# Kernel optimization log

Measured on AMD Instinct MI355X. Metric: run time of the kernel, lower is better.

## Reference

```python
import jax, jax.numpy as jnp
import numpy as np
from jax import lax

IMAGE_SIZE = 512
MIN_LEVEL, MAX_LEVEL = 3, 7
NUM_SCALES = 3
RATIOS = (1.0, 0.5, 2.0)
BASE_SCALE = 4
PRE_NMS = 5000
POST_NMS = 100
IOU_THR = 0.5
SCORE_THR = 0.2
NUM_CLASSES = 90
BATCH = 8


def _anchors():
    """Multiscale anchors [N,4] in (y1,x1,y2,x2) pixel coords, N=49104 for 512."""
    all_boxes = []
    for level in range(MIN_LEVEL, MAX_LEVEL + 1):
        stride = 2 ** level
        feat = IMAGE_SIZE // stride
        cy = (np.arange(feat, dtype=np.float32) + 0.5) * stride
        cx = (np.arange(feat, dtype=np.float32) + 0.5) * stride
        yv, xv = np.meshgrid(cy, cx, indexing='ij')
        yv = yv.reshape(-1)
        xv = xv.reshape(-1)
        half = []  # (half_h, half_w) per anchor config, 9 per cell
        for i in range(NUM_SCALES):
            base = (2.0 ** (i / 3.0)) * stride * BASE_SCALE
            for r in RATIOS:
                half.append((base / np.sqrt(r) / 2.0, base * np.sqrt(r) / 2.0))
        half = np.asarray(half, dtype=np.float32)  # [9,2]
        boxes = np.stack([
            yv[:, None] - half[None, :, 0],
            xv[:, None] - half[None, :, 1],
            yv[:, None] + half[None, :, 0],
            xv[:, None] + half[None, :, 1],
        ], axis=-1)  # [feat*feat, 9, 4]
        all_boxes.append(boxes.reshape(-1, 4))
    return np.concatenate(all_boxes, axis=0).astype(np.float32)


def setup_inputs() -> dict:
    key = jax.random.key(0)
    k1, k2 = jax.random.split(key)
    n = 49104
    box_deltas = jax.random.normal(k1, (BATCH, n, 4), jnp.float32) * 0.1
    cls_logits = jax.random.normal(k2, (BATCH, n, NUM_CLASSES), jnp.float32)
    return {"box_deltas": box_deltas, "cls_logits": cls_logits}


def _decode(anchors, deltas):
    # Delta2Box with mean=None/std=None: standard (dy,dx,dh,dw) decode.
    ah = anchors[:, 2] - anchors[:, 0]
    aw = anchors[:, 3] - anchors[:, 1]
    acy = (anchors[:, 0] + anchors[:, 2]) * 0.5
    acx = (anchors[:, 1] + anchors[:, 3]) * 0.5
    dy, dx, dh, dw = deltas[..., 0], deltas[..., 1], deltas[..., 2], deltas[..., 3]
    cy = dy * ah + acy
    cx = dx * aw + acx
    h = jnp.exp(dh) * ah
    w = jnp.exp(dw) * aw
    return jnp.stack([cy - h * 0.5, cx - w * 0.5, cy + h * 0.5, cx + w * 0.5], axis=-1)


def _iou_one_many(box, boxes):
    yy1 = jnp.maximum(box[0], boxes[:, 0])
    xx1 = jnp.maximum(box[1], boxes[:, 1])
    yy2 = jnp.minimum(box[2], boxes[:, 2])
    xx2 = jnp.minimum(box[3], boxes[:, 3])
    inter = jnp.maximum(yy2 - yy1, 0.0) * jnp.maximum(xx2 - xx1, 0.0)
    a1 = (box[2] - box[0]) * (box[3] - box[1])
    a2 = (boxes[:, 2] - boxes[:, 0]) * (boxes[:, 3] - boxes[:, 1])
    return inter / (a1 + a2 - inter + 1e-8)


def _nms_single(boxes, scores):
    # Greedy NMS over K boxes, at most POST_NMS selections. boxes [K,4], scores [K].
    @jax.checkpoint
    def step(s, _):
        i = jnp.argmax(s)
        sc = s[i]
        b = boxes[i]
        valid = sc > SCORE_THR
        suppress = _iou_one_many(b, boxes) > IOU_THR  # includes self
        s = jnp.where(suppress, jnp.float32(-1.0), s)
        out_b = jnp.where(valid, b, jnp.zeros_like(b))
        out_s = jnp.where(valid, sc, jnp.float32(0.0))
        return s, (out_b, out_s)
    _, (sel_b, sel_s) = lax.scan(step, scores, None, length=POST_NMS)
    return sel_b, sel_s  # [POST,4], [POST]


def reference(box_deltas, cls_logits):
    anchors = jnp.asarray(_anchors())
    boxes = _decode(anchors, box_deltas)                      # [B,N,4]
    boxes = jnp.clip(boxes / jnp.float32(IMAGE_SIZE), 0.0, 1.0)
    scores = jax.nn.sigmoid(cls_logits)                       # [B,N,C]
    scores_t = jnp.swapaxes(scores, 1, 2)                     # [B,C,N]
    top_s, top_i = lax.top_k(scores_t, PRE_NMS)               # [B,C,K]
    B = boxes.shape[0]
    bidx = jnp.arange(B)[:, None, None]
    top_b = boxes[bidx, top_i]                                # [B,C,K,4]
    sel_b, sel_s = jax.vmap(jax.vmap(_nms_single))(top_b, top_s)  # [B,C,P,4],[B,C,P]
    cls_ids = jnp.broadcast_to(
        jnp.arange(NUM_CLASSES, dtype=jnp.float32)[None, :, None], sel_s.shape)
    flat_s = sel_s.reshape(B, -1)
    flat_b = sel_b.reshape(B, -1, 4)
    flat_c = cls_ids.reshape(B, -1)
    out_s, idx = lax.top_k(flat_s, POST_NMS)                  # combine over classes
    bi = jnp.arange(B)[:, None]
    out_b = flat_b[bi, idx]
    out_c = flat_c[bi, idx]
    valid = jnp.sum((out_s > 0).astype(jnp.int32), axis=1)
    return out_b, out_s, out_c, valid
```

## Files before the change

kernel.cpp:

```cpp
#include <hip/hip_runtime.h>
#include <math.h>


#define NANCH 49104
#define NB 8
#define NC 90
#define NBC 720
#define POSTN 100
#define T1CAP 512
#define WMAX 8
#define CHUNK 512
#define NCH 96
#define LCAP 32
#define EDGE 0.93f
#define PRECHK 2.0f


__device__ __forceinline__ float sigmoid_ref(float x) {
  if (x >= 0.0f) return __fdiv_rn(1.0f, __fadd_rn(1.0f, expf(-x)));
  float e = expf(x);
  return __fdiv_rn(e, __fadd_rn(1.0f, e));
}

__device__ __forceinline__ float iou_ref(float4 a, float4 b) {
  float yy1 = fmaxf(a.x, b.x);
  float xx1 = fmaxf(a.y, b.y);
  float yy2 = fminf(a.z, b.z);
  float xx2 = fminf(a.w, b.w);
  float ih = fmaxf(__fsub_rn(yy2, yy1), 0.0f);
  float iw = fmaxf(__fsub_rn(xx2, xx1), 0.0f);
  float inter = __fmul_rn(ih, iw);
  float a1 = __fmul_rn(__fsub_rn(a.z, a.x), __fsub_rn(a.w, a.y));
  float a2 = __fmul_rn(__fsub_rn(b.z, b.x), __fsub_rn(b.w, b.y));
  float den = __fadd_rn(__fsub_rn(__fadd_rn(a1, a2), inter), 1e-8f);
  return __fdiv_rn(inter, den);
}


__global__ __launch_bounds__(256) void k_anchors(float4* __restrict__ anchors,
                                                 unsigned int* __restrict__ gcnt,
                                                 unsigned int* __restrict__ oflow) {
  int n = blockIdx.x * 256 + threadIdx.x;
  if (n < NBC) { gcnt[n] = 0u; oflow[n] = 0u; }
  if (n >= NANCH) return;
  int l, off;
  if (n < 36864)      { l = 0; off = 0; }
  else if (n < 46080) { l = 1; off = 36864; }
  else if (n < 48384) { l = 2; off = 46080; }
  else if (n < 48960) { l = 3; off = 48384; }
  else                { l = 4; off = 48960; }
  int stride = 8 << l;
  int feat = 64 >> l;
  int r = n - off;
  int cell = r / 9, a = r - cell * 9;
  int iy = cell / feat, ix = cell - iy * feat;
  int isc = a / 3, ir = a - isc * 3;
  double base = exp2((double)isc / 3.0) * (double)stride * 4.0;
  double rt = (ir == 0) ? 1.0 : (ir == 1 ? 0.5 : 2.0);
  double sq = sqrt(rt);
  float hh = (float)(base / sq / 2.0);
  float hw = (float)(base * sq / 2.0);
  float cy = __fmul_rn(__fadd_rn((float)iy, 0.5f), (float)stride);
  float cx = __fmul_rn(__fadd_rn((float)ix, 0.5f), (float)stride);
  anchors[n] = make_float4(__fsub_rn(cy, hh), __fsub_rn(cx, hw),
                           __fadd_rn(cy, hh), __fadd_rn(cx, hw));
}


__global__ __launch_bounds__(256) void k_decode(const float4* __restrict__ deltas,
                                                const float4* __restrict__ anchors,
                                                float4* __restrict__ boxes) {
  int i = blockIdx.x * 256 + threadIdx.x;
  if (i >= NB * NANCH) return;
  int n = i % NANCH;
  float4 a = anchors[n];
  float4 d = deltas[i];
  float ah = __fsub_rn(a.z, a.x);
  float aw = __fsub_rn(a.w, a.y);
  float acy = __fmul_rn(__fadd_rn(a.x, a.z), 0.5f);
  float acx = __fmul_rn(__fadd_rn(a.y, a.w), 0.5f);
  float cy = __fadd_rn(__fmul_rn(d.x, ah), acy);
  float cx = __fadd_rn(__fmul_rn(d.y, aw), acx);
  float h = __fmul_rn(expf(d.z), ah);
  float w = __fmul_rn(expf(d.w), aw);
  float y1 = __fsub_rn(cy, __fmul_rn(h, 0.5f));
  float x1 = __fsub_rn(cx, __fmul_rn(w, 0.5f));
  float y2 = __fadd_rn(cy, __fmul_rn(h, 0.5f));
  float x2 = __fadd_rn(cx, __fmul_rn(w, 0.5f));
  const float inv = 0.001953125f;
  y1 = fminf(fmaxf(__fmul_rn(y1, inv), 0.0f), 1.0f);
  x1 = fminf(fmaxf(__fmul_rn(x1, inv), 0.0f), 1.0f);
  y2 = fminf(fmaxf(__fmul_rn(y2, inv), 0.0f), 1.0f);
  x2 = fminf(fmaxf(__fmul_rn(x2, inv), 0.0f), 1.0f);
  boxes[i] = make_float4(y1, x1, y2, x2);
}


__global__ __launch_bounds__(256) void k_scan(const float4* __restrict__ logits4,
                                              unsigned long long* __restrict__ gcand,
                                              unsigned int* __restrict__ gcnt,
                                              unsigned int* __restrict__ oflow) {
  int b = blockIdx.y;
  int ch = blockIdx.x;
  int n0 = ch * CHUNK;
  int rows = min(CHUNK, NANCH - n0);
  const float4* base = logits4 + ((size_t)b * NANCH + n0) * 90 / 4;
  int tot4 = rows * 90 / 4;
  int tid = threadIdx.x;

  __shared__ unsigned long long lc[NC * LCAP];
  __shared__ unsigned int lcnt[NC];
  for (int c = tid; c < NC; c += 256) lcnt[c] = 0u;
  __syncthreads();

  for (int e4 = tid; e4 < tot4; e4 += 1024) {
    float4 v[4];
#pragma unroll
    for (int k = 0; k < 4; k++) {
      int idx = e4 + k * 256;
      if (idx < tot4) v[k] = base[idx];
    }
#pragma unroll
    for (int k = 0; k < 4; k++) {
      int idx = e4 + k * 256;
      if (idx >= tot4) break;
      float xs[4] = {v[k].x, v[k].y, v[k].z, v[k].w};
#pragma unroll
      for (int j = 0; j < 4; j++) {
        float x = xs[j];
        if (x >= PRECHK) {
          float s = sigmoid_ref(x);
          if (s >= EDGE) {
            int e = idx * 4 + j;
            int r = e / 90, c = e - r * 90;
            unsigned int pos = atomicAdd(&lcnt[c], 1u);
            if (pos < LCAP) {
              int n = n0 + r;
              lc[c * LCAP + pos] =
                  ((unsigned long long)__float_as_uint(s) << 32) |
                  (unsigned int)(65535 - n);
            }
          }
        }
      }
    }
  }
  __syncthreads();

  if (tid < NC) {
    unsigned int cnt = lcnt[tid];
    int bc = b * NC + tid;
    if (cnt > LCAP) {
      atomicOr(&oflow[bc], 1u);
      cnt = LCAP;
    }
    if (cnt > 0) {
      unsigned int pos0 = atomicAdd(&gcnt[bc], cnt);
      for (unsigned int k = 0; k < cnt; k++) {
        unsigned int p = pos0 + k;
        if (p < T1CAP) gcand[(size_t)bc * T1CAP + p] = lc[tid * LCAP + k];
      }
    }
  }
}


__global__ __launch_bounds__(256) void k_nms_t1(
    const unsigned long long* __restrict__ gcand,
    const unsigned int* __restrict__ gcnt, const unsigned int* __restrict__ oflow,
    const float4* __restrict__ boxes, float* __restrict__ sel_s,
    float4* __restrict__ sel_b, int* __restrict__ flags) {
  int bc = blockIdx.x;
  int b = bc / NC;
  int tid = threadIdx.x;
  int lane = tid & 63;
  int wv = tid >> 6;

  __shared__ unsigned long long cand[T1CAP];
  __shared__ float4 cbox[T1CAP];
  __shared__ __align__(16) unsigned long long rowm[T1CAP][WMAX];
  __shared__ int s_seli[POSTN];
  __shared__ int s_nsel;

  unsigned int cnt = gcnt[bc];
  bool overflow = (cnt > (unsigned)T1CAP) || (oflow[bc] != 0u);
  int M = (int)min(cnt, (unsigned)T1CAP);
  for (int e = tid; e < T1CAP; e += 256)
    cand[e] = (e < M) ? gcand[(size_t)bc * T1CAP + e] : 0ull;
  if (tid == 0) s_nsel = 0;
  __syncthreads();

  int SN = (M <= 128) ? 128 : (M <= 256) ? 256 : 512;
  int np = SN >> 1;
  for (int k = 2; k <= SN; k <<= 1) {
    for (int j = k >> 1; j > 0; j >>= 1) {
      int t = tid;
      if (t < np) {
        int i = ((t & ~(j - 1)) << 1) | (t & (j - 1));
        int p = i | j;
        unsigned long long a = cand[i], bb = cand[p];
        bool up = ((i & k) == 0);
        if (up ? (a < bb) : (a > bb)) { cand[i] = bb; cand[p] = a; }
      }
      __syncthreads();
    }
  }

  for (int e = tid; e < T1CAP; e += 256) {
    if (e < M) {
      int n = 65535 - (int)(cand[e] & 0xFFFFull);
      cbox[e] = boxes[(size_t)b * NANCH + n];
    } else {
      cbox[e] = make_float4(0.0f, 0.0f, 0.0f, 0.0f);
    }
  }
  __syncthreads();

  int W = (M + 63) >> 6;

  for (int i = tid; i < M; i += 256) {
    float4 bi = cbox[i];
    int wi = i >> 6;
    unsigned int bl = (unsigned int)(i & 63);
#pragma unroll
    for (int w = 0; w < WMAX; w++) {
      unsigned long long acc = 0ull;
      if (w >= wi && w < W) {
        int jmax = min(64, M - (w << 6));
#pragma unroll 4
        for (int jj = 0; jj < jmax; jj++) {
          float4 bj = cbox[(w << 6) + jj];
          if (iou_ref(bj, bi) > 0.5f) acc |= (1ull << jj);
        }
        if (w == wi) acc &= (~0ull) << bl;
      }
      rowm[i][w] = acc;
    }
  }
  __syncthreads();

  if (wv == 0) {
    unsigned long long av[WMAX];
#pragma unroll
    for (int w = 0; w < WMAX; w++) {
      int lo = w << 6;
      av[w] = (M >= lo + 64) ? ~0ull
            : (M > lo ? ((1ull << (M - lo)) - 1ull) : 0ull);
    }
    int nsel = 0;
    int pidx = -1;
    unsigned long long pr[WMAX];
#pragma unroll
    for (int w = 0; w < WMAX; w++) pr[w] = 0ull;
    for (int p = 0; p < POSTN; p++) {
      int idx = -1;
#pragma unroll
      for (int w = 0; w < WMAX; w++) {
        if (idx < 0 && av[w] != 0ull)
          idx = (w << 6) + (__ffsll((unsigned long long)av[w]) - 1);
      }
      if (idx < 0) break;
      if (lane == 0) s_seli[p] = idx;
      nsel++;
      if (idx == pidx) {
#pragma unroll
        for (int w = 0; w < WMAX; w++) av[w] &= ~pr[w];
      } else {
        const ulonglong2* rp = (const ulonglong2*)(&rowm[idx][0]);
#pragma unroll
        for (int w = 0; w < 4; w++) {
          ulonglong2 rr = rp[w];
          av[2 * w] &= ~rr.x;
          av[2 * w + 1] &= ~rr.y;
        }
      }
      int nx = idx + 1;
      if (nx < M) {
        const ulonglong2* rp2 = (const ulonglong2*)(&rowm[nx][0]);
#pragma unroll
        for (int w = 0; w < 4; w++) {
          ulonglong2 rr = rp2[w];
          pr[2 * w] = rr.x;
          pr[2 * w + 1] = rr.y;
        }
        pidx = nx;
      } else {
        pidx = -1;
      }
    }
    if (lane == 0) s_nsel = nsel;
  }
  __syncthreads();

  int ns = s_nsel;
  bool bad = overflow || (ns < POSTN);
  if (tid == 0) flags[bc] = bad ? 1 : 0;
  if (bad) return;
  for (int p = tid; p < POSTN; p += 256) {
    int i = s_seli[p];
    float s0 = __uint_as_float((unsigned int)(cand[i] >> 32));
    float4 bx = cbox[i];
    bool valid = (s0 > 0.2f);
    sel_s[bc * POSTN + p] = valid ? s0 : 0.0f;
    sel_b[bc * POSTN + p] = valid ? bx : make_float4(0, 0, 0, 0);
  }
}


__global__ __launch_bounds__(256) void k_flagall(int* __restrict__ flags) {
  int i = blockIdx.x * 256 + threadIdx.x;
  if (i < NBC) flags[i] = 1;
}


template <int CAP, int RANK>
__global__ __launch_bounds__(256) void k_nms_fb(const float* __restrict__ logits,
                                                const float4* __restrict__ boxes,
                                                float* __restrict__ sel_s,
                                                float4* __restrict__ sel_b,
                                                const int* __restrict__ flags) {
  int bc = blockIdx.x;
  if (flags[bc] == 0) return;
  int b = bc / NC;
  int c = bc - b * NC;
  int tid = threadIdx.x;

  __shared__ unsigned int s_key[CAP];
  __shared__ unsigned short s_idx[CAP];
  __shared__ __align__(16) unsigned char s_pool[8192];
  __shared__ unsigned int s_bsum[256];
  __shared__ unsigned char s_alive[512];
  __shared__ float4 s_selbox[POSTN];
  __shared__ float s_sels[POSTN];
  __shared__ int s_cnt, s_nsel, s_cutbin;

  const float* lrow = logits + (size_t)b * NANCH * 90 + c;

  unsigned int* hist = (unsigned int*)s_pool;
  for (int e = tid; e < 2048; e += 256) hist[e] = 0u;
  if (tid == 0) { s_cnt = 0; s_nsel = 0; s_cutbin = 0; }
  __syncthreads();

  for (int n = tid; n < NANCH; n += 256) {
    float s = sigmoid_ref(lrow[(size_t)n * 90]);
    int bin = (int)(s * 2048.0f);
    if (bin > 2047) bin = 2047;
    atomicAdd(&hist[bin], 1u);
  }
  __syncthreads();
  unsigned int loc = 0;
#pragma unroll
  for (int k = 0; k < 8; k++) loc += hist[tid * 8 + k];
  s_bsum[tid] = loc;
  __syncthreads();
  if (tid == 0) {
    unsigned int cum = 0;
    int bin = 0;
    bool fnd = false;
    for (int t = 255; t >= 0 && !fnd; t--) {
      if (cum + s_bsum[t] >= (unsigned)RANK) {
        for (int kk = 7; kk >= 0; kk--) {
          unsigned int h = hist[t * 8 + kk];
          if (cum + h >= (unsigned)RANK) { bin = t * 8 + kk; fnd = true; break; }
          cum += h;
        }
      } else {
        cum += s_bsum[t];
      }
    }
    s_cutbin = bin;
  }
  __syncthreads();
  float edge = __fmul_rn((float)s_cutbin, (1.0f / 2048.0f));

  for (int n = tid; n < NANCH; n += 256) {
    float s = sigmoid_ref(lrow[(size_t)n * 90]);
    if (s >= edge) {
      int pos = atomicAdd(&s_cnt, 1);
      if (pos < CAP) {
        s_key[pos] = __float_as_uint(s);
        s_idx[pos] = (unsigned short)n;
      }
    }
  }
  __syncthreads();
  int M = s_cnt;
  if (M > CAP) M = CAP;
  for (int e = M + tid; e < CAP; e += 256) { s_key[e] = 0u; s_idx[e] = 0xFFFFu; }
  __syncthreads();

  for (int k = 2; k <= CAP; k <<= 1) {
    for (int j = k >> 1; j > 0; j >>= 1) {
      for (int t = tid; t < CAP / 2; t += 256) {
        int i = ((t & ~(j - 1)) << 1) | (t & (j - 1));
        int p = i | j;
        unsigned int ka = s_key[i], kb = s_key[p];
        unsigned short ia = s_idx[i], ib = s_idx[p];
        bool up = ((i & k) == 0);
        bool g = (ka < kb) || (ka == kb && ia > ib);
        bool l = (kb < ka) || (ka == kb && ib > ia);
        if (up ? g : l) {
          s_key[i] = kb; s_key[p] = ka;
          s_idx[i] = ib; s_idx[p] = ia;
        }
      }
      __syncthreads();
    }
  }

  float4* cbox = (float4*)s_pool;
  int L = (M < 5000) ? M : 5000;
  for (int base = 0; base < L; base += 512) {
    int cn = min(512, L - base);
    int ns0 = s_nsel;
    if (ns0 >= POSTN) break;
    for (int t = tid; t < cn; t += 256) {
      int n = s_idx[base + t];
      float4 bx = boxes[(size_t)b * NANCH + n];
      bool al = true;
      for (int s = 0; s < ns0; s++) {
        if (iou_ref(bx, s_selbox[s]) > 0.5f) { al = false; break; }
      }
      cbox[t] = bx;
      s_alive[t] = al ? 1 : 0;
    }
    __syncthreads();
    for (int i = 0; i < cn; i++) {
      if (s_nsel >= POSTN) break;
      if (!s_alive[i]) continue;
      float4 bi = cbox[i];
      float sc = __uint_as_float(s_key[base + i]);
      if (!(iou_ref(bi, bi) > 0.5f)) {
        if (tid == 0) {
          for (int p = s_nsel; p < POSTN; p++) { s_selbox[p] = bi; s_sels[p] = sc; }
          s_nsel = POSTN;
        }
        __syncthreads();
        break;
      }
      for (int t = tid; t < cn; t += 256) {
        if (t > i && s_alive[t] && iou_ref(cbox[t], bi) > 0.5f) s_alive[t] = 0;
      }
      if (tid == 0) {
        s_selbox[s_nsel] = bi;
        s_sels[s_nsel] = sc;
        s_nsel = s_nsel + 1;
      }
      __syncthreads();
    }
    __syncthreads();
    if (s_nsel >= POSTN) break;
  }
  __syncthreads();
  int ns = s_nsel;
  for (int p = tid; p < POSTN; p += 256) {
    float sc = 0.0f;
    float4 bx = make_float4(0.0f, 0.0f, 0.0f, 0.0f);
    if (p < ns) {
      float s0 = s_sels[p];
      if (s0 > 0.2f) { sc = s0; bx = s_selbox[p]; }
    }
    sel_s[bc * POSTN + p] = sc;
    sel_b[bc * POSTN + p] = bx;
  }
}


__global__ __launch_bounds__(64) void k_final(const float* __restrict__ sel_s,
                                              const float4* __restrict__ sel_b,
                                              float* __restrict__ out) {
  int b = blockIdx.x;
  int tid = threadIdx.x;
  __shared__ float key[9000];
  __shared__ unsigned int win_k[POSTN];
  __shared__ int win_e[POSTN];
  for (int e = tid; e < 9000; e += 64) key[e] = sel_s[(size_t)b * 9000 + e];
  int p0 = 0, p1 = 0;
  int c1 = tid + 64;
  __syncthreads();
  for (int p = 0; p < POSTN; p++) {
    unsigned long long v = 0ull;
    if (p0 < POSTN) {
      int e = tid * POSTN + p0;
      v = ((unsigned long long)__float_as_uint(key[e]) << 32) |
          (unsigned int)(16383 - e);
    }
    if (c1 < NC && p1 < POSTN) {
      int e = c1 * POSTN + p1;
      unsigned long long v2 = ((unsigned long long)__float_as_uint(key[e]) << 32) |
                              (unsigned int)(16383 - e);
      if (v2 > v) v = v2;
    }
#pragma unroll
    for (int d = 1; d < 64; d <<= 1) {
      unsigned long long o = __shfl_xor(v, d, 64);
      if (o > v) v = o;
    }
    int e = 16383 - (int)(v & 0x3FFFull);
    if (tid == 0) { win_k[p] = (unsigned int)(v >> 32); win_e[p] = e; }
    int cls = e / POSTN;
    int pp = e - cls * POSTN;
    if (cls == tid) p0 = pp + 1;
    else if (cls == c1) p1 = pp + 1;
  }
  __syncthreads();
  for (int p = tid; p < POSTN; p += 64) {
    unsigned int k = win_k[p];
    int e = win_e[p];
    float4 bx = sel_b[(size_t)b * 9000 + e];
    ((float4*)out)[b * POSTN + p] = bx;
    out[3200 + b * POSTN + p] = __uint_as_float(k);
    out[4000 + b * POSTN + p] = (float)(e / POSTN);
  }
  int vcnt = 0;
  for (int p = tid; p < POSTN; p += 64) vcnt += (win_k[p] != 0u) ? 1 : 0;
#pragma unroll
  for (int d = 1; d < 64; d <<= 1) vcnt += __shfl_xor(vcnt, d, 64);
  if (tid == 0) out[4800 + b] = (float)vcnt;
}


extern "C" void kernel_launch(void* const* d_in, const int* in_sizes, int n_in,
                              void* d_out, int out_size, void* d_ws, size_t ws_size,
                              hipStream_t stream) {
  const float* deltas = (const float*)d_in[0];
  const float* logits = (const float*)d_in[1];
  float* out = (float*)d_out;
  char* ws = (char*)d_ws;

  size_t off = 0;
  auto take = [&](size_t bytes) -> char* {
    char* p = ws + off;
    off += (bytes + 255) & ~(size_t)255;
    return p;
  };
  float4* anchors = (float4*)take((size_t)NANCH * 16);
  float4* boxes = (float4*)take((size_t)NB * NANCH * 16);
  float* sel_s = (float*)take((size_t)NBC * POSTN * 4);
  float4* sel_b = (float4*)take((size_t)NBC * POSTN * 16);
  int* flags = (int*)take((size_t)NBC * 4);
  unsigned int* gcnt = (unsigned int*)take((size_t)NBC * 4);
  unsigned int* oflow = (unsigned int*)take((size_t)NBC * 4);
  unsigned long long* gcand =
      (unsigned long long*)take((size_t)NBC * T1CAP * 8);
  bool fits = (off <= ws_size);

  k_anchors<<<dim3((NANCH + 255) / 256), dim3(256), 0, stream>>>(anchors, gcnt,
                                                                 oflow);
  k_decode<<<dim3((NB * NANCH + 255) / 256), dim3(256), 0, stream>>>(
      (const float4*)deltas, anchors, boxes);
  if (fits) {
    k_scan<<<dim3(NCH, NB), dim3(256), 0, stream>>>((const float4*)logits,
                                                    gcand, gcnt, oflow);
    k_nms_t1<<<dim3(NBC), dim3(256), 0, stream>>>(gcand, gcnt, oflow, boxes,
                                                  sel_s, sel_b, flags);
  } else {
    k_flagall<<<dim3((NBC + 255) / 256), dim3(256), 0, stream>>>(flags);
  }
  k_nms_fb<8192, 5000><<<dim3(NBC), dim3(256), 0, stream>>>(logits, boxes,
                                                            sel_s, sel_b, flags);
  k_final<<<dim3(NB), dim3(64), 0, stream>>>(sel_s, sel_b, out);
}
```

Baseline: 344.5 us.

## Batch self-only NMS selections and replace k_final merge with histogram top-k

In the tier-1 NMS kernel, each row records via ballot whether the box suppresses nothing except itself. The greedy loop then selects runs of such boxes in bulk, without reading the mask rows one candidate at a time. The final cross-class merge, previously 100 serial 64-lane argmax rounds, becomes a 256-thread histogram threshold on score bits, a compaction of candidates above the cutoff, and a bitonic sort. The old serial merge remains as a fallback when more than 512 candidates pass the cutoff. The aim is to shorten the serial critical path in both kernels, at the cost of more code and shared-memory atomics.

```diff
diff --git a/kernel.cpp b/kernel.cpp
--- a/kernel.cpp
+++ b/kernel.cpp
@@ -179,6 +179,7 @@
   __shared__ unsigned long long cand[T1CAP];
   __shared__ float4 cbox[T1CAP];
   __shared__ __align__(16) unsigned long long rowm[T1CAP][WMAX];
+  __shared__ unsigned long long sonly[WMAX];
   __shared__ int s_seli[POSTN];
   __shared__ int s_nsel;
 
@@ -188,6 +189,7 @@
   for (int e = tid; e < T1CAP; e += 256)
     cand[e] = (e < M) ? gcand[(size_t)bc * T1CAP + e] : 0ull;
   if (tid == 0) s_nsel = 0;
+  if (tid < WMAX) sonly[tid] = 0ull;
   __syncthreads();
 
   int SN = (M <= 128) ? 128 : (M <= 256) ? 256 : 512;
@@ -222,6 +224,7 @@
     float4 bi = cbox[i];
     int wi = i >> 6;
     unsigned int bl = (unsigned int)(i & 63);
+    bool so = true;
 #pragma unroll
     for (int w = 0; w < WMAX; w++) {
       unsigned long long acc = 0ull;
@@ -235,7 +238,10 @@
         if (w == wi) acc &= (~0ull) << bl;
       }
       rowm[i][w] = acc;
-    }
+      so = so && (acc == ((w == wi) ? (1ull << bl) : 0ull));
+    }
+    unsigned long long bal = __ballot((int)so);
+    if (lane == 0) sonly[i >> 6] = bal;
   }
   __syncthreads();
 
@@ -247,45 +253,35 @@
       av[w] = (M >= lo + 64) ? ~0ull
             : (M > lo ? ((1ull << (M - lo)) - 1ull) : 0ull);
     }
+    unsigned long long sor[WMAX];
+#pragma unroll
+    for (int w = 0; w < WMAX; w++) sor[w] = sonly[w];
     int nsel = 0;
-    int pidx = -1;
-    unsigned long long pr[WMAX];
-#pragma unroll
-    for (int w = 0; w < WMAX; w++) pr[w] = 0ull;
-    for (int p = 0; p < POSTN; p++) {
-      int idx = -1;
-#pragma unroll
-      for (int w = 0; w < WMAX; w++) {
-        if (idx < 0 && av[w] != 0ull)
-          idx = (w << 6) + (__ffsll((unsigned long long)av[w]) - 1);
-      }
-      if (idx < 0) break;
-      if (lane == 0) s_seli[p] = idx;
-      nsel++;
-      if (idx == pidx) {
-#pragma unroll
-        for (int w = 0; w < WMAX; w++) av[w] &= ~pr[w];
+    while (nsel < POSTN) {
+      int w = -1;
+#pragma unroll
+      for (int ww = 0; ww < WMAX; ww++)
+        if (w < 0 && av[ww] != 0ull) w = ww;
+      if (w < 0) break;
+      unsigned long long m = av[w];
+      unsigned long long bad = m & ~sor[w];
+      unsigned long long pre =
+          bad ? (m & ((bad & (0ull - bad)) - 1ull)) : m;
+      if (pre != 0ull) {
+        while (pre != 0ull && nsel < POSTN) {
+          int bit = __ffsll((unsigned long long)pre) - 1;
+          if (lane == 0) s_seli[nsel] = (w << 6) + bit;
+          nsel++;
+          pre &= pre - 1ull;
+          av[w] &= ~(1ull << bit);
+        }
       } else {
-        const ulonglong2* rp = (const ulonglong2*)(&rowm[idx][0]);
-#pragma unroll
-        for (int w = 0; w < 4; w++) {
-          ulonglong2 rr = rp[w];
-          av[2 * w] &= ~rr.x;
-          av[2 * w + 1] &= ~rr.y;
-        }
-      }
-      int nx = idx + 1;
-      if (nx < M) {
-        const ulonglong2* rp2 = (const ulonglong2*)(&rowm[nx][0]);
-#pragma unroll
-        for (int w = 0; w < 4; w++) {
-          ulonglong2 rr = rp2[w];
-          pr[2 * w] = rr.x;
-          pr[2 * w + 1] = rr.y;
-        }
-        pidx = nx;
-      } else {
-        pidx = -1;
+        int bit = __ffsll((unsigned long long)m) - 1;
+        int idx = (w << 6) + bit;
+        if (lane == 0) s_seli[nsel] = idx;
+        nsel++;
+#pragma unroll
+        for (int ww = 0; ww < WMAX; ww++) av[ww] &= ~rowm[idx][ww];
       }
     }
     if (lane == 0) s_nsel = nsel;
@@ -466,45 +462,136 @@
 }
 
 
-__global__ __launch_bounds__(64) void k_final(const float* __restrict__ sel_s,
-                                              const float4* __restrict__ sel_b,
-                                              float* __restrict__ out) {
+__global__ __launch_bounds__(256) void k_final(const float* __restrict__ sel_s,
+                                               const float4* __restrict__ sel_b,
+                                               float* __restrict__ out) {
   int b = blockIdx.x;
   int tid = threadIdx.x;
-  __shared__ float key[9000];
+  __shared__ __align__(16) unsigned char pool[36864];
   __shared__ unsigned int win_k[POSTN];
   __shared__ int win_e[POSTN];
-  for (int e = tid; e < 9000; e += 64) key[e] = sel_s[(size_t)b * 9000 + e];
-  int p0 = 0, p1 = 0;
-  int c1 = tid + 64;
-  __syncthreads();
-  for (int p = 0; p < POSTN; p++) {
-    unsigned long long v = 0ull;
-    if (p0 < POSTN) {
-      int e = tid * POSTN + p0;
-      v = ((unsigned long long)__float_as_uint(key[e]) << 32) |
-          (unsigned int)(16383 - e);
-    }
-    if (c1 < NC && p1 < POSTN) {
-      int e = c1 * POSTN + p1;
-      unsigned long long v2 = ((unsigned long long)__float_as_uint(key[e]) << 32) |
-                              (unsigned int)(16383 - e);
-      if (v2 > v) v = v2;
-    }
-#pragma unroll
-    for (int d = 1; d < 64; d <<= 1) {
-      unsigned long long o = __shfl_xor(v, d, 64);
-      if (o > v) v = o;
-    }
-    int e = 16383 - (int)(v & 0x3FFFull);
-    if (tid == 0) { win_k[p] = (unsigned int)(v >> 32); win_e[p] = e; }
-    int cls = e / POSTN;
-    int pp = e - cls * POSTN;
-    if (cls == tid) p0 = pp + 1;
-    else if (cls == c1) p1 = pp + 1;
-  }
-  __syncthreads();
-  for (int p = tid; p < POSTN; p += 64) {
+  __shared__ unsigned int csum[256];
+  __shared__ int s_cut, s_cnt;
+
+  const float* srow = sel_s + (size_t)b * 9000;
+  unsigned int* hist = (unsigned int*)pool;
+  unsigned long long* ckey = (unsigned long long*)(pool + 16384);
+
+  for (int e = tid; e < 4096; e += 256) hist[e] = 0u;
+  if (tid == 0) s_cnt = 0;
+  __syncthreads();
+
+  for (int e = tid; e < 9000; e += 256) {
+    unsigned int bits = __float_as_uint(srow[e]);
+    int bin = (bits >= 0x3F000000u)
+                  ? min(4095, (int)(2048u + ((bits - 0x3F000000u) >> 12)))
+                  : (int)(bits >> 20);
+    atomicAdd(&hist[bin], 1u);
+  }
+  __syncthreads();
+
+  unsigned int loc = 0;
+#pragma unroll
+  for (int k = 0; k < 16; k++) loc += hist[tid * 16 + k];
+  csum[tid] = loc;
+  __syncthreads();
+
+  if (tid == 0) {
+    unsigned int cum = 0;
+    int cut = 0;
+    bool fnd = false;
+    for (int t = 255; t >= 0 && !fnd; t--) {
+      if (cum + csum[t] >= (unsigned)POSTN) {
+        for (int kk = 15; kk >= 0; kk--) {
+          int bn = t * 16 + kk;
+          unsigned int h = hist[bn];
+          if (cum + h >= (unsigned)POSTN) { cut = bn; fnd = true; break; }
+          cum += h;
+        }
+      } else {
+        cum += csum[t];
+      }
+    }
+    s_cut = cut;
+  }
+  __syncthreads();
+  int cut = s_cut;
+
+  for (int e = tid; e < 9000; e += 256) {
+    unsigned int bits = __float_as_uint(srow[e]);
+    int bin = (bits >= 0x3F000000u)
+                  ? min(4095, (int)(2048u + ((bits - 0x3F000000u) >> 12)))
+                  : (int)(bits >> 20);
+    if (bin >= cut) {
+      int pos = atomicAdd(&s_cnt, 1);
+      if (pos < 512)
+        ckey[pos] = ((unsigned long long)bits << 32) | (unsigned int)(16383 - e);
+    }
+  }
+  __syncthreads();
+  int cnt = s_cnt;
+
+  if (cnt <= 512) {
+    int SN = (cnt <= 256) ? 256 : 512;
+    for (int e = tid; e < SN; e += 256)
+      if (e >= cnt) ckey[e] = 0ull;
+    __syncthreads();
+    for (int k = 2; k <= SN; k <<= 1) {
+      for (int j = k >> 1; j > 0; j >>= 1) {
+        int t = tid;
+        if (t < (SN >> 1)) {
+          int i = ((t & ~(j - 1)) << 1) | (t & (j - 1));
+          int p = i | j;
+          unsigned long long a = ckey[i], bb = ckey[p];
+          bool up = ((i & k) == 0);
+          if (up ? (a < bb) : (a > bb)) { ckey[i] = bb; ckey[p] = a; }
+        }
+        __syncthreads();
+      }
+    }
+    if (tid < POSTN) {
+      unsigned long long v = ckey[tid];
+      win_k[tid] = (unsigned int)(v >> 32);
+      win_e[tid] = 16383 - (int)(v & 0x3FFFull);
+    }
+  } else {
+    float* key = (float*)pool;
+    int* ptr = (int*)(pool + 36032);
+    unsigned long long* wred = (unsigned long long*)(pool + 36416);
+    for (int e = tid; e < 9000; e += 256) key[e] = srow[e];
+    if (tid < NC) ptr[tid] = 0;
+    __syncthreads();
+    int lane = tid & 63, wid = tid >> 6;
+    for (int p = 0; p < POSTN; p++) {
+      unsigned long long v = 0ull;
+      if (tid < NC) {
+        int pp = ptr[tid];
+        if (pp < POSTN) {
+          int e = tid * POSTN + pp;
+          v = ((unsigned long long)__float_as_uint(key[e]) << 32) |
+              (unsigned int)(16383 - e);
+        }
+      }
+      for (int d = 32; d > 0; d >>= 1) {
+        unsigned long long o = __shfl_down(v, (unsigned)d, 64);
+        if (o > v) v = o;
+      }
+      if (lane == 0) wred[wid] = v;
+      __syncthreads();
+      if (tid == 0) {
+        unsigned long long w2 = wred[0];
+        if (wred[1] > w2) w2 = wred[1];
+        int e = 16383 - (int)(w2 & 0x3FFFull);
+        win_k[p] = (unsigned int)(w2 >> 32);
+        win_e[p] = e;
+        ptr[e / POSTN] = (e % POSTN) + 1;
+      }
+      __syncthreads();
+    }
+  }
+  __syncthreads();
+
+  for (int p = tid; p < POSTN; p += 256) {
     unsigned int k = win_k[p];
     int e = win_e[p];
     float4 bx = sel_b[(size_t)b * 9000 + e];
@@ -512,11 +599,11 @@
     out[3200 + b * POSTN + p] = __uint_as_float(k);
     out[4000 + b * POSTN + p] = (float)(e / POSTN);
   }
-  int vcnt = 0;
-  for (int p = tid; p < POSTN; p += 64) vcnt += (win_k[p] != 0u) ? 1 : 0;
-#pragma unroll
-  for (int d = 1; d < 64; d <<= 1) vcnt += __shfl_xor(vcnt, d, 64);
-  if (tid == 0) out[4800 + b] = (float)vcnt;
+  if (tid == 0) {
+    int v = 0;
+    for (int p = 0; p < POSTN; p++) v += (win_k[p] != 0u) ? 1 : 0;
+    out[4800 + b] = (float)v;
+  }
 }
 
 
@@ -559,5 +646,5 @@
   }
   k_nms_fb<8192, 5000><<<dim3(NBC), dim3(256), 0, stream>>>(logits, boxes,
                                                             sel_s, sel_b, flags);
-  k_final<<<dim3(NB), dim3(64), 0, stream>>>(sel_s, sel_b, out);
-}
+  k_final<<<dim3(NB), dim3(256), 0, stream>>>(sel_s, sel_b, out);
+}
```

Result: faster. 323.4 us (-6.1%).
